# Optimization experiments

Measured on AMD Instinct MI355X. Metric: run time of the kernel, lower is better.

The kernel has to match this reference:

```python
import jax, jax.numpy as jnp
import numpy as np

N, E, B = 20000, 320000, 64
HID, DEPTH, NFREQ = 128, 4, 8
NODE_DIM, EDGE_DIM, SG = 4, 3, 230
TWO_PI = 2.0 * np.pi


def setup_inputs() -> dict:
    key = jax.random.key(0)
    ks = jax.random.split(key, 20)
    inp = {}
    inp["x"] = jax.random.normal(ks[0], (N, NODE_DIM), jnp.float32)
    inp["edge_index"] = jax.random.randint(ks[1], (2, E), 0, N)
    inp["edge_attr"] = jax.random.normal(ks[2], (E, EDGE_DIM), jnp.float32)
    inp["batch"] = jnp.sort(jax.random.randint(ks[3], (N,), 0, B))
    inp["space_group"] = jax.random.randint(ks[4], (B,), 0, SG)
    inp["node_w"] = jax.random.normal(ks[5], (NODE_DIM, HID), jnp.float32) * 0.1
    inp["node_b"] = jnp.zeros((HID,), jnp.float32)
    inp["sg_table"] = jax.random.normal(ks[6], (SG, HID), jnp.float32) * 0.1
    inp["lin_w"] = jax.random.normal(ks[7], (DEPTH, 2 * HID + EDGE_DIM, HID), jnp.float32) * 0.05
    inp["lin_b"] = jnp.zeros((DEPTH, HID), jnp.float32)
    inp["att_w"] = jax.random.normal(ks[8], (DEPTH, 2 * HID + EDGE_DIM), jnp.float32) * 0.05
    inp["att_b"] = jnp.zeros((DEPTH,), jnp.float32)
    inp["fk_w"] = jax.random.normal(ks[9], (DEPTH, NFREQ, HID, HID), jnp.float32) * 0.1
    inp["fk_b"] = jnp.zeros((DEPTH, HID), jnp.float32)
    inp["bn_g"] = jnp.ones((DEPTH, HID), jnp.float32)
    inp["bn_b"] = jnp.zeros((DEPTH, HID), jnp.float32)
    inp["pool_w"] = jax.random.normal(ks[10], (HID,), jnp.float32) * 0.1
    inp["pool_b"] = jnp.zeros((), jnp.float32)
    inp["head_w1"] = jax.random.normal(ks[11], (4, 2 * HID, HID), jnp.float32) * 0.05
    inp["head_b1"] = jnp.zeros((4, HID), jnp.float32)
    for i, (nm, od) in enumerate([("e", 1), ("s", 3), ("c", 7), ("m", 3)]):
        inp[nm + "_w2"] = jax.random.normal(ks[12 + i], (HID, od), jnp.float32) * 0.05
        inp[nm + "_b2"] = jnp.zeros((od,), jnp.float32)
    return inp


def reference(x, edge_index, edge_attr, batch, space_group, node_w, node_b, sg_table,
              lin_w, lin_b, att_w, att_b, fk_w, fk_b, bn_g, bn_b, pool_w, pool_b,
              head_w1, head_b1, e_w2, e_b2, s_w2, s_b2, c_w2, c_b2, m_w2, m_b2):
    src, dst = edge_index[0], edge_index[1]  # x_j = x[src], x_i = x[dst]
    h = x @ node_w + node_b                  # [N, HID]
    sg = sg_table[space_group]               # [B, HID]
    freqs = jnp.arange(1, NFREQ + 1, dtype=h.dtype)
    for l in range(DEPTH):
        # edge conv: gather-concat-linear-sigmoid attention-scatter add
        tmp = jnp.concatenate([h[dst], h[src], edge_attr], axis=-1)   # [E, 2H+3]
        alpha = jax.nn.sigmoid(tmp @ att_w[l] + att_b[l])[:, None]    # [E, 1]
        msg = alpha * (tmp @ lin_w[l] + lin_b[l])                     # [E, H]
        h_conv = jax.ops.segment_sum(msg, dst, num_segments=N)
        # Fourier-Kolmogorov branch
        ang = TWO_PI * freqs[None, :, None] * h[:, None, :]           # [N, K, H]
        h_fk = (jnp.einsum('nki,kio->no', jnp.sin(ang), fk_w[l])
                + jnp.einsum('nki,kio->no', jnp.cos(ang), fk_w[l]) + fk_b[l])
        h = h_conv + h_fk
        # BatchNorm1d (batch statistics, training semantics) + ReLU; dropout = identity (eval)
        mu = h.mean(axis=0)
        var = h.var(axis=0)
        h = (h - mu) / jnp.sqrt(var + 1e-5) * bn_g[l] + bn_b[l]
        h = jax.nn.relu(h)
    # attention pool: softmax over ALL nodes (dim=0), as in the original
    a = jax.nn.softmax(h @ pool_w + pool_b, axis=0)[:, None]          # [N, 1]
    pooled = jax.ops.segment_sum(a * h, batch, num_segments=B)        # [B, H]
    comb = jnp.concatenate([pooled, sg], axis=-1)                     # [B, 2H]

    def head(i, w2, b2):
        z = jax.nn.relu(comb @ head_w1[i] + head_b1[i])
        return z @ w2 + b2

    energy = head(0, e_w2, e_b2)          # [B, 1]
    stability = head(1, s_w2, s_b2)       # [B, 3]
    crystal_system = head(2, c_w2, c_b2)  # [B, 7]
    material_type = head(3, m_w2, m_b2)   # [B, 3]
    return energy, stability, crystal_system, material_type
```

## Files before the change

kernel.cpp:

```cpp
#include <hip/hip_runtime.h>
#include <math.h>

#define HID 128
#define DEPTH 4
#define PSPLIT 16
#define SMAXB 40

typedef _Float16 half8 __attribute__((ext_vector_type(8)));
typedef float f4 __attribute__((ext_vector_type(4)));

__global__ void k_wsplit(const float* __restrict__ fkw, _Float16* __restrict__ whi,
                         _Float16* __restrict__ wlo) {
    __shared__ float sh[64][65];
    int bid = blockIdx.x;
    int l = bid >> 5; int r = bid & 31; int kb = r >> 1; int nbk = r & 1;
    const float* W = fkw + (size_t)l * 131072;
    _Float16* Hl = whi + (size_t)l * 131072;
    _Float16* Ll = wlo + (size_t)l * 131072;
    int k0 = kb * 64, n0 = nbk * 64;
    for (int i = threadIdx.x; i < 4096; i += 256) {
        int kk = i >> 6, nn = i & 63;
        sh[kk][nn] = W[(k0 + kk) * HID + n0 + nn];
    }
    __syncthreads();
    for (int i = threadIdx.x; i < 4096; i += 256) {
        int nn = i >> 6, kk = i & 63;
        float w = sh[kk][nn];
        _Float16 hi = (_Float16)w;
        _Float16 lo = (_Float16)((w - (float)hi) * 2048.f);
        Hl[(n0 + nn) * 1024 + k0 + kk] = hi;
        Ll[(n0 + nn) * 1024 + k0 + kk] = lo;
    }
}

__global__ void k_wsplit2(const float* __restrict__ linw, _Float16* __restrict__ lwhi,
                          _Float16* __restrict__ lwlo) {
    __shared__ float sh[64][65];
    int bid = blockIdx.x;
    int l = bid >> 3; int r = bid & 7; int cb = r >> 1; int kb = r & 1;
    const float* W = linw + (size_t)l * 259 * HID;
    int c0 = cb * 64, k0 = kb * 64;
    const float* base = W + (size_t)((c0 >= 128) ? 128 : 0) * HID + (c0 & 127);
    for (int i = threadIdx.x; i < 4096; i += 256) {
        int kk = i >> 6, cc = i & 63;
        sh[kk][cc] = base[(size_t)(k0 + kk) * HID + cc];
    }
    __syncthreads();
    _Float16* Hl = lwhi + (size_t)l * 32768;
    _Float16* Ll = lwlo + (size_t)l * 32768;
    for (int i = threadIdx.x; i < 4096; i += 256) {
        int cc = i >> 6, kk = i & 63;
        float w = sh[kk][cc];
        _Float16 hi = (_Float16)w;
        _Float16 lo = (_Float16)((w - (float)hi) * 2048.f);
        Hl[(size_t)(c0 + cc) * 128 + k0 + kk] = hi;
        Ll[(size_t)(c0 + cc) * 128 + k0 + kk] = lo;
    }
}

__global__ void k_hist(const int* __restrict__ dst, int* __restrict__ deg, int E) {
    int e = blockIdx.x * 256 + threadIdx.x;
    if (e < E) atomicAdd(&deg[dst[e]], 1);
}

__global__ void k_scan_a(const int* __restrict__ deg, int* __restrict__ bsum, int N) {
    __shared__ int sh[256];
    int i = blockIdx.x * 256 + threadIdx.x;
    sh[threadIdx.x] = (i < N) ? deg[i] : 0;
    __syncthreads();
    for (int off = 128; off > 0; off >>= 1) {
        if (threadIdx.x < (unsigned)off) sh[threadIdx.x] += sh[threadIdx.x + off];
        __syncthreads();
    }
    if (threadIdx.x == 0) bsum[blockIdx.x] = sh[0];
}

__global__ void k_scan_b(int* __restrict__ bsum, int nb) {
    __shared__ int sh[256];
    int v = (threadIdx.x < (unsigned)nb) ? bsum[threadIdx.x] : 0;
    sh[threadIdx.x] = v;
    __syncthreads();
    for (int off = 1; off < 256; off <<= 1) {
        int add = (threadIdx.x >= (unsigned)off) ? sh[threadIdx.x - off] : 0;
        __syncthreads();
        sh[threadIdx.x] += add;
        __syncthreads();
    }
    if (threadIdx.x < (unsigned)nb) bsum[threadIdx.x] = sh[threadIdx.x] - v;
}

__global__ void k_scan_c(const int* __restrict__ deg, const int* __restrict__ bsum,
                         int* __restrict__ offs, int* __restrict__ cursor, int N) {
    __shared__ int sh[256];
    int i = blockIdx.x * 256 + threadIdx.x;
    int v = (i < N) ? deg[i] : 0;
    sh[threadIdx.x] = v;
    __syncthreads();
    for (int off = 1; off < 256; off <<= 1) {
        int add = (threadIdx.x >= (unsigned)off) ? sh[threadIdx.x - off] : 0;
        __syncthreads();
        sh[threadIdx.x] += add;
        __syncthreads();
    }
    int ex = bsum[blockIdx.x] + sh[threadIdx.x] - v;
    if (i < N) { offs[i] = ex; cursor[i] = ex; }
    if (i == N - 1) offs[N] = ex + v;
}

__global__ void k_scatter(const int* __restrict__ src, const int* __restrict__ dst,
                          const float* __restrict__ ea, int* cursor,
                          int* __restrict__ srco, float4* __restrict__ ea3o, int E) {
    int e = blockIdx.x * 256 + threadIdx.x;
    if (e < E) {
        int d = dst[e];
        int p = atomicAdd(&cursor[d], 1);
        srco[p] = src[e];
        float4 q;
        q.x = ea[e * 3 + 0]; q.y = ea[e * 3 + 1]; q.z = ea[e * 3 + 2]; q.w = 0.f;
        ea3o[p] = q;
    }
}

__global__ void k_bstart(const int* __restrict__ batch, int* __restrict__ boffs, int N, int B) {
    int n = blockIdx.x * 256 + threadIdx.x;
    if (n >= N) return;
    int b1 = batch[n];
    if (n == 0) for (int b = 0; b <= b1; ++b) boffs[b] = 0;
    int b2 = (n + 1 < N) ? batch[n + 1] : B;
    for (int b = b1 + 1; b <= b2; ++b) boffs[b] = n + 1;
}

__global__ __launch_bounds__(512, 4) void k_nlgemm(const float* __restrict__ hsrc,
        const float* __restrict__ x, const float* __restrict__ nw, const float* __restrict__ nbv,
        const double* __restrict__ bnst, const float* __restrict__ bng, const float* __restrict__ bnb,
        int mode,
        const _Float16* __restrict__ lwhi, const _Float16* __restrict__ lwlo,
        const float* __restrict__ linb,
        const float* __restrict__ attw, const float* __restrict__ attb,
        float* __restrict__ A1, float* __restrict__ A2,
        float* __restrict__ a1, float* __restrict__ a2, int N) {
    __shared__ _Float16 ahi[32 * 128];
    __shared__ _Float16 alo[32 * 128];
    __shared__ float s_sc[128], s_sh[128];
    int tid = threadIdx.x;
    int nb = blockIdx.x * 32;
    if (mode == 1) {
        if (tid < 128) {
            double invN = 1.0 / (double)N;
            float mu = (float)(bnst[tid] * invN);
            float var = (float)(bnst[128 + tid] * invN) - mu * mu;
            float inv = 1.f / sqrtf(var + 1e-5f);
            float sc = bng[tid] * inv;
            s_sc[tid] = sc;
            s_sh[tid] = bnb[tid] - mu * sc;
        }
        __syncthreads();
    }
    {
        int row = tid >> 4;
        int o16 = tid & 15;
        int gn = nb + row;
        int rc = (gn < N) ? gn : (N - 1);
        float hv[8];
        if (mode == 0) {
            float4 xr = *(const float4*)&x[(size_t)rc * 4];
#pragma unroll
            for (int j = 0; j < 8; ++j) {
                int c = o16 * 8 + j;
                hv[j] = nbv[c] + xr.x * nw[c] + xr.y * nw[HID + c]
                       + xr.z * nw[2 * HID + c] + xr.w * nw[3 * HID + c];
            }
        } else {
            const float* hp = hsrc + (size_t)rc * HID + o16 * 8;
            *(float4*)&hv[0] = *(const float4*)hp;
            *(float4*)&hv[4] = *(const float4*)(hp + 4);
#pragma unroll
            for (int j = 0; j < 8; ++j) {
                int c = o16 * 8 + j;
                hv[j] = fmaxf(hv[j] * s_sc[c] + s_sh[c], 0.f);
            }
        }
        float p1 = 0.f, p2 = 0.f;
#pragma unroll
        for (int j = 0; j < 8; ++j) {
            int k = o16 * 8 + j;
            p1 += hv[j] * attw[k];
            p2 += hv[j] * attw[128 + k];
        }
        for (int off = 8; off > 0; off >>= 1) {
            p1 += __shfl_down(p1, off, 16);
            p2 += __shfl_down(p2, off, 16);
        }
        if (o16 == 0 && gn < N) {
            a1[gn] = p1 + attb[0];
            a2[gn] = p2;
        }
        int rs = row & 7;
        half8 vh, vl;
#pragma unroll
        for (int j = 0; j < 8; ++j) {
            float a = hv[j];
            _Float16 hi = (_Float16)a;
            vh[j] = hi;
            vl[j] = (_Float16)((a - (float)hi) * 2048.f);
        }
        int oct = o16 ^ rs;
        *(half8*)&ahi[row * 128 + oct * 8] = vh;
        *(half8*)&alo[row * 128 + oct * 8] = vl;
    }
    __syncthreads();
    int lane = tid & 63, wv = tid >> 6;
    int quad = lane >> 4, l16 = lane & 15;
    int n0 = wv * 32;
    f4 acc0[2][2], accL[2][2];
#pragma unroll
    for (int mi = 0; mi < 2; ++mi)
#pragma unroll
        for (int ni = 0; ni < 2; ++ni) { acc0[mi][ni] = (f4)(0.f); accL[mi][ni] = (f4)(0.f); }
    const _Float16* bhp0 = lwhi + (size_t)(n0 + l16) * 128 + quad * 8;
    const _Float16* bhp1 = lwhi + (size_t)(n0 + 16 + l16) * 128 + quad * 8;
    const _Float16* blp0 = lwlo + (size_t)(n0 + l16) * 128 + quad * 8;
    const _Float16* blp1 = lwlo + (size_t)(n0 + 16 + l16) * 128 + quad * 8;
    int rs16 = (l16 & 7) << 3;
#pragma unroll
    for (int step = 0; step < 4; ++step) {
        int ka = (step * 32 + quad * 8) ^ rs16;
        int ko = step * 32;
        half8 bh0 = *(const half8*)(bhp0 + ko);
        half8 bh1 = *(const half8*)(bhp1 + ko);
        half8 bl0 = *(const half8*)(blp0 + ko);
        half8 bl1 = *(const half8*)(blp1 + ko);
        half8 ah[2], al[2];
#pragma unroll
        for (int mi = 0; mi < 2; ++mi) {
            ah[mi] = *(const half8*)&ahi[(l16 + mi * 16) * 128 + ka];
            al[mi] = *(const half8*)&alo[(l16 + mi * 16) * 128 + ka];
        }
#pragma unroll
        for (int mi = 0; mi < 2; ++mi) {
            acc0[mi][0] = __builtin_amdgcn_mfma_f32_16x16x32_f16(ah[mi], bh0, acc0[mi][0], 0, 0, 0);
            acc0[mi][1] = __builtin_amdgcn_mfma_f32_16x16x32_f16(ah[mi], bh1, acc0[mi][1], 0, 0, 0);
            accL[mi][0] = __builtin_amdgcn_mfma_f32_16x16x32_f16(ah[mi], bl0, accL[mi][0], 0, 0, 0);
            accL[mi][1] = __builtin_amdgcn_mfma_f32_16x16x32_f16(ah[mi], bl1, accL[mi][1], 0, 0, 0);
            accL[mi][0] = __builtin_amdgcn_mfma_f32_16x16x32_f16(al[mi], bh0, accL[mi][0], 0, 0, 0);
            accL[mi][1] = __builtin_amdgcn_mfma_f32_16x16x32_f16(al[mi], bh1, accL[mi][1], 0, 0, 0);
        }
    }
    const float inv = 1.0f / 2048.0f;
#pragma unroll
    for (int mi = 0; mi < 2; ++mi)
#pragma unroll
        for (int ni = 0; ni < 2; ++ni)
#pragma unroll
            for (int r = 0; r < 4; ++r) {
                int gn = nb + mi * 16 + quad * 4 + r;
                if (gn >= N) continue;
                int cp = n0 + ni * 16 + l16;
                float val = acc0[mi][ni][r] + accL[mi][ni][r] * inv;
                if (cp < 128) A1[(size_t)gn * HID + cp] = val + linb[cp];
                else          A2[(size_t)gn * HID + cp - 128] = val;
            }
}

__global__ __launch_bounds__(256) void k_edge(const float* __restrict__ A1,
        const float* __restrict__ A2, const float* __restrict__ a1,
        const float* __restrict__ a2, const int* __restrict__ srco,
        const float4* __restrict__ ea3o, const int* __restrict__ offs,
        const float* __restrict__ linw3, const float* __restrict__ attw3,
        float* __restrict__ hconv, int N) {
    __shared__ float part[8][HID + 4];
    int n = blockIdx.x;
    int tid = threadIdx.x;
    int lane32 = tid & 31, slot = tid >> 5;
    int c4 = lane32 * 4;
    float4 w0v = *(const float4*)&linw3[c4];
    float4 w1v = *(const float4*)&linw3[HID + c4];
    float4 w2v = *(const float4*)&linw3[2 * HID + c4];
    float aw0 = attw3[0], aw1 = attw3[1], aw2 = attw3[2];
    float a1n = a1[n];
    float4 A1v = *(const float4*)&A1[(size_t)n * HID + c4];
    float4 acc; acc.x = acc.y = acc.z = acc.w = 0.f;
    int s0 = offs[n], s1 = offs[n + 1];
    for (int idx = s0 + slot; idx < s1; idx += 8) {
        int s = srco[idx];
        float4 q = ea3o[idx];
        float logit = a1n + a2[s] + q.x * aw0 + q.y * aw1 + q.z * aw2;
        float al = 1.f / (1.f + __expf(-logit));
        float4 a2v = *(const float4*)&A2[(size_t)s * HID + c4];
        float4 pre;
        pre.x = A1v.x + a2v.x + q.x * w0v.x + q.y * w1v.x + q.z * w2v.x;
        pre.y = A1v.y + a2v.y + q.x * w0v.y + q.y * w1v.y + q.z * w2v.y;
        pre.z = A1v.z + a2v.z + q.x * w0v.z + q.y * w1v.z + q.z * w2v.z;
        pre.w = A1v.w + a2v.w + q.x * w0v.w + q.y * w1v.w + q.z * w2v.w;
        acc.x += al * pre.x; acc.y += al * pre.y;
        acc.z += al * pre.z; acc.w += al * pre.w;
    }
    *(float4*)&part[slot][c4] = acc;
    __syncthreads();
    if (slot == 0) {
        float4 p = *(const float4*)&part[0][c4];
#pragma unroll
        for (int s = 1; s < 8; ++s) {
            float4 r = *(const float4*)&part[s][c4];
            p.x += r.x; p.y += r.y; p.z += r.z; p.w += r.w;
        }
        *(float4*)&hconv[(size_t)n * HID + c4] = p;
    }
}

#define FK_MT 64
__global__ __launch_bounds__(512, 4) void k_fk(const float* __restrict__ hsrc,
        const float* __restrict__ x, const float* __restrict__ nw, const float* __restrict__ nbv,
        const double* __restrict__ bnst, const float* __restrict__ bng, const float* __restrict__ bnb,
        int mode,
        const _Float16* __restrict__ whi, const _Float16* __restrict__ wlo,
        float* __restrict__ p0, float* __restrict__ p1,
        float* __restrict__ p2, float* __restrict__ p3, int N) {
    __shared__ _Float16 ahi[FK_MT * 256];
    __shared__ _Float16 alo[FK_MT * 256];
    __shared__ float s_sc[128], s_sh[128];
    int tid = threadIdx.x;
    int bx = blockIdx.x;
    int nb = (bx >> 2) * FK_MT;
    int ks = bx & 3;
    int kbase = ks * 256;
    int fr0 = kbase >> 7;
    if (mode == 1) {
        if (tid < 128) {
            double invN = 1.0 / (double)N;
            float mu = (float)(bnst[tid] * invN);
            float var = (float)(bnst[128 + tid] * invN) - mu * mu;
            float inv = 1.f / sqrtf(var + 1e-5f);
            float sc = bng[tid] * inv;
            s_sc[tid] = sc;
            s_sh[tid] = bnb[tid] - mu * sc;
        }
        __syncthreads();
    }
    {
        int row = tid >> 3;
        int o8 = tid & 7;
        int gn = nb + row;
        int rc = (gn < N) ? gn : (N - 1);
        float hv[2][8];
        if (mode == 0) {
            float4 xr = *(const float4*)&x[(size_t)rc * 4];
#pragma unroll
            for (int s = 0; s < 2; ++s)
#pragma unroll
                for (int j = 0; j < 8; ++j) {
                    int c = s * 64 + o8 * 8 + j;
                    hv[s][j] = nbv[c] + xr.x * nw[c] + xr.y * nw[HID + c]
                              + xr.z * nw[2 * HID + c] + xr.w * nw[3 * HID + c];
                }
        } else {
            const float* hp = hsrc + (size_t)rc * HID + o8 * 8;
            *(float4*)&hv[0][0] = *(const float4*)hp;
            *(float4*)&hv[0][4] = *(const float4*)(hp + 4);
            *(float4*)&hv[1][0] = *(const float4*)(hp + 64);
            *(float4*)&hv[1][4] = *(const float4*)(hp + 68);
#pragma unroll
            for (int s = 0; s < 2; ++s)
#pragma unroll
                for (int j = 0; j < 8; ++j) {
                    int c = s * 64 + o8 * 8 + j;
                    hv[s][j] = fmaxf(hv[s][j] * s_sc[c] + s_sh[c], 0.f);
                }
        }
        int rs = row & 7;
#pragma unroll
        for (int g = 0; g < 2; ++g) {
            float freqf = 6.2831853f * (float)(fr0 + g + 1);
#pragma unroll
            for (int s = 0; s < 2; ++s) {
                half8 vh, vl;
#pragma unroll
                for (int j = 0; j < 8; ++j) {
                    float ang = freqf * hv[s][j] + 0.78539816f;
                    float a = 1.41421356f * __sinf(ang);
                    _Float16 hi = (_Float16)a;
                    vh[j] = hi;
                    vl[j] = (_Float16)((a - (float)hi) * 2048.f);
                }
                int oct = (g * 16 + s * 8 + o8) ^ rs;
                *(half8*)&ahi[row * 256 + oct * 8] = vh;
                *(half8*)&alo[row * 256 + oct * 8] = vl;
            }
        }
    }
    __syncthreads();
    int lane = tid & 63, wv = tid >> 6;
    int quad = lane >> 4, l16 = lane & 15;
    int n0w = wv * 16;
    f4 acc0[4], accL[4];
#pragma unroll
    for (int mi = 0; mi < 4; ++mi) { acc0[mi] = (f4)(0.f); accL[mi] = (f4)(0.f); }
    const _Float16* bhp = whi + (size_t)(n0w + l16) * 1024 + kbase + quad * 8;
    const _Float16* blp = wlo + (size_t)(n0w + l16) * 1024 + kbase + quad * 8;
    int rs16 = (l16 & 7) << 3;
#pragma unroll 2
    for (int step = 0; step < 8; ++step) {
        int ka = (step * 32 + quad * 8) ^ rs16;
        int ko = step * 32;
        half8 bh = *(const half8*)(bhp + ko);
        half8 bl = *(const half8*)(blp + ko);
        half8 ah[4], al[4];
#pragma unroll
        for (int mi = 0; mi < 4; ++mi) {
            ah[mi] = *(const half8*)&ahi[(l16 + mi * 16) * 256 + ka];
            al[mi] = *(const half8*)&alo[(l16 + mi * 16) * 256 + ka];
        }
#pragma unroll
        for (int mi = 0; mi < 4; ++mi) {
            acc0[mi] = __builtin_amdgcn_mfma_f32_16x16x32_f16(ah[mi], bh, acc0[mi], 0, 0, 0);
            accL[mi] = __builtin_amdgcn_mfma_f32_16x16x32_f16(ah[mi], bl, accL[mi], 0, 0, 0);
            accL[mi] = __builtin_amdgcn_mfma_f32_16x16x32_f16(al[mi], bh, accL[mi], 0, 0, 0);
        }
    }
    float* p = (ks == 0) ? p0 : (ks == 1) ? p1 : (ks == 2) ? p2 : p3;
    const float inv = 1.0f / 2048.0f;
#pragma unroll
    for (int mi = 0; mi < 4; ++mi)
#pragma unroll
        for (int r = 0; r < 4; ++r) {
            int gn = nb + mi * 16 + quad * 4 + r;
            if (gn < N)
                p[gn * HID + n0w + l16] = acc0[mi][r] + accL[mi][r] * inv;
        }
}

__global__ __launch_bounds__(256) void k_bn_stats(float* __restrict__ hconv,
                           const float* __restrict__ p0, const float* __restrict__ p1,
                           const float* __restrict__ p2, const float* __restrict__ p3,
                           const float* __restrict__ fkb,
                           double* __restrict__ stats, int N) {
    int tid = threadIdx.x;
    int cq = tid & 31, rg = tid >> 5;
    int c4 = cq * 4;
    float4 bias = *(const float4*)&fkb[c4];
    float s1[4] = {0, 0, 0, 0}, s2[4] = {0, 0, 0, 0};
    for (int n = blockIdx.x * 8 + rg; n < N; n += gridDim.x * 8) {
        size_t idx = (size_t)n * HID + c4;
        float4 a  = *(const float4*)&hconv[idx];
        float4 b0 = *(const float4*)&p0[idx];
        float4 b1 = *(const float4*)&p1[idx];
        float4 b2 = *(const float4*)&p2[idx];
        float4 b3 = *(const float4*)&p3[idx];
        float4 v;
        v.x = a.x + b0.x + b1.x + b2.x + b3.x + bias.x;
        v.y = a.y + b0.y + b1.y + b2.y + b3.y + bias.y;
        v.z = a.z + b0.z + b1.z + b2.z + b3.z + bias.z;
        v.w = a.w + b0.w + b1.w + b2.w + b3.w + bias.w;
        *(float4*)&hconv[idx] = v;
        s1[0] += v.x; s2[0] += v.x * v.x;
        s1[1] += v.y; s2[1] += v.y * v.y;
        s1[2] += v.z; s2[2] += v.z * v.z;
        s1[3] += v.w; s2[3] += v.w * v.w;
    }
#pragma unroll
    for (int j = 0; j < 4; ++j) {
        s1[j] += __shfl_down(s1[j], 32);
        s2[j] += __shfl_down(s2[j], 32);
    }
    __shared__ float sh1[4][32][4], sh2[4][32][4];
    int wv = tid >> 6, lane = tid & 63;
    if (lane < 32) {
#pragma unroll
        for (int j = 0; j < 4; ++j) { sh1[wv][lane][j] = s1[j]; sh2[wv][lane][j] = s2[j]; }
    }
    __syncthreads();
    if (tid < 128) {
        int cq2 = tid >> 2, j2 = tid & 3;
        float t1 = sh1[0][cq2][j2] + sh1[1][cq2][j2] + sh1[2][cq2][j2] + sh1[3][cq2][j2];
        float t2 = sh2[0][cq2][j2] + sh2[1][cq2][j2] + sh2[2][cq2][j2] + sh2[3][cq2][j2];
        int c = cq2 * 4 + j2;
        atomicAdd(&stats[c], (double)t1);
        atomicAdd(&stats[128 + c], (double)t2);
    }
}

__global__ void k_bn_apply(const float* __restrict__ hsum, const double* __restrict__ stats,
                           const float* __restrict__ g, const float* __restrict__ b,
                           const float* __restrict__ pw, const float* __restrict__ pb,
                           float* __restrict__ h, float* __restrict__ s,
                           int do_score, int N) {
    int idx = blockIdx.x * 256 + threadIdx.x;
    int row = idx >> 5, cq = idx & 31;
    int c4 = cq * 4;
    int valid = row < N;
    double invN = 1.0 / (double)N;
    float p = 0.f;
    if (valid) {
        float4 hv = *(const float4*)&hsum[(size_t)row * HID + c4];
        float vin[4] = {hv.x, hv.y, hv.z, hv.w};
        float4 ov;
        float* po = &ov.x;
#pragma unroll
        for (int j = 0; j < 4; ++j) {
            int c = c4 + j;
            float mu = (float)(stats[c] * invN);
            float var = (float)(stats[128 + c] * invN) - mu * mu;
            float inv = 1.f / sqrtf(var + 1e-5f);
            float sc = g[c] * inv;
            float sh = b[c] - mu * sc;
            float oo = fmaxf(vin[j] * sc + sh, 0.f);
            po[j] = oo;
            if (do_score) p += oo * pw[c];
        }
        *(float4*)&h[(size_t)row * HID + c4] = ov;
    }
    if (do_score) {
        for (int off = 16; off > 0; off >>= 1) p += __shfl_down(p, off, 32);
        if ((threadIdx.x & 31) == 0 && valid) s[row] = p + pb[0];
    }
}

__global__ void k_smax1(const float* __restrict__ s, float* __restrict__ mzp, int N) {
    __shared__ float red[256];
    float m = -INFINITY;
    for (int n = blockIdx.x * 256 + threadIdx.x; n < N; n += SMAXB * 256)
        m = fmaxf(m, s[n]);
    red[threadIdx.x] = m;
    __syncthreads();
    for (int off = 128; off > 0; off >>= 1) {
        if (threadIdx.x < (unsigned)off)
            red[threadIdx.x] = fmaxf(red[threadIdx.x], red[threadIdx.x + off]);
        __syncthreads();
    }
    m = red[0];
    __syncthreads();
    float z = 0.f;
    for (int n = blockIdx.x * 256 + threadIdx.x; n < N; n += SMAXB * 256)
        z += __expf(s[n] - m);
    red[threadIdx.x] = z;
    __syncthreads();
    for (int off = 128; off > 0; off >>= 1) {
        if (threadIdx.x < (unsigned)off) red[threadIdx.x] += red[threadIdx.x + off];
        __syncthreads();
    }
    if (threadIdx.x == 0) { mzp[blockIdx.x * 2] = m; mzp[blockIdx.x * 2 + 1] = red[0]; }
}

__device__ __forceinline__ void combine_mz(const float* mzp, float& m, float& Z) {
    m = -INFINITY;
#pragma unroll 8
    for (int i = 0; i < SMAXB; ++i) m = fmaxf(m, mzp[i * 2]);
    Z = 0.f;
#pragma unroll 8
    for (int i = 0; i < SMAXB; ++i) Z += mzp[i * 2 + 1] * __expf(mzp[i * 2] - m);
}

__global__ void k_pool_part(const float* __restrict__ h, const float* __restrict__ s,
                            const float* __restrict__ mzp, const int* __restrict__ boffs,
                            float* __restrict__ part) {
    int b = blockIdx.x >> 4, split = blockIdx.x & (PSPLIT - 1);
    int c = threadIdx.x & 127, half = threadIdx.x >> 7;
    float m, Z;
    combine_mz(mzp, m, Z);
    (void)Z;
    int n0 = boffs[b], n1 = boffs[b + 1];
    float acc = 0.f;
    for (int n = n0 + split * 2 + half; n < n1; n += PSPLIT * 2)
        acc += __expf(s[n] - m) * h[n * HID + c];
    __shared__ float prt[2][HID];
    prt[half][c] = acc;
    __syncthreads();
    if (half == 0) part[(size_t)(b * PSPLIT + split) * HID + c] = prt[0][c] + prt[1][c];
}

__global__ void k_pool_sum(const float* __restrict__ part, const float* __restrict__ mzp,
                           float* __restrict__ pooled) {
    int b = blockIdx.x, c = threadIdx.x;
    float m, Z;
    combine_mz(mzp, m, Z);
    float acc = 0.f;
#pragma unroll
    for (int i = 0; i < PSPLIT; ++i) acc += part[(size_t)(b * PSPLIT + i) * HID + c];
    pooled[b * HID + c] = acc / Z;
}

__global__ __launch_bounds__(256) void k_head(const float* __restrict__ pooled,
                       const float* __restrict__ sg_table,
                       const int* __restrict__ space_group,
                       const float* __restrict__ hw1, const float* __restrict__ hb1,
                       const float* __restrict__ ew2, const float* __restrict__ eb2,
                       const float* __restrict__ sw2, const float* __restrict__ sb2,
                       const float* __restrict__ cw2, const float* __restrict__ cb2,
                       const float* __restrict__ mw2, const float* __restrict__ mb2,
                       float* __restrict__ out, int B) {
    __shared__ float comb[256];
    __shared__ float zred[2][128];
    __shared__ float zsh[128];
    int b = blockIdx.x >> 2, i = blockIdx.x & 3;
    int t = threadIdx.x;
    comb[t] = (t < 128) ? pooled[b * HID + t] : sg_table[space_group[b] * HID + (t - 128)];
    __syncthreads();
    int half = t >> 7, tt = t & 127;
    const float* W = hw1 + ((size_t)i * 256 + half * 128) * HID;
    const float* cb = &comb[half * 128];
    float z = 0.f;
#pragma unroll 8
    for (int k = 0; k < 128; ++k) z += cb[k] * W[k * HID + tt];
    zred[half][tt] = z;
    __syncthreads();
    if (t < 128) zsh[t] = fmaxf(zred[0][t] + zred[1][t] + hb1[i * HID + t], 0.f);
    __syncthreads();
    const int od[4] = {1, 3, 7, 3};
    const int base[4] = {0, 64, 256, 704};
    const float* w2 = (i == 0) ? ew2 : (i == 1) ? sw2 : (i == 2) ? cw2 : mw2;
    const float* b2 = (i == 0) ? eb2 : (i == 1) ? sb2 : (i == 2) ? cb2 : mb2;
    int odi = od[i];
    if (t < odi) {
        float o = b2[t];
        for (int c = 0; c < HID; ++c) o += zsh[c] * w2[c * odi + t];
        out[base[i] + b * odi + t] = o;
    }
}

extern "C" void kernel_launch(void* const* d_in, const int* in_sizes, int n_in,
                              void* d_out, int out_size, void* d_ws, size_t ws_size,
                              hipStream_t stream) {
    const float* x          = (const float*)d_in[0];
    const int*   edge_index = (const int*)d_in[1];
    const float* edge_attr  = (const float*)d_in[2];
    const int*   batch      = (const int*)d_in[3];
    const int*   space_group= (const int*)d_in[4];
    const float* node_w     = (const float*)d_in[5];
    const float* node_b     = (const float*)d_in[6];
    const float* sg_table   = (const float*)d_in[7];
    const float* lin_w      = (const float*)d_in[8];
    const float* lin_b      = (const float*)d_in[9];
    const float* att_w      = (const float*)d_in[10];
    const float* att_b      = (const float*)d_in[11];
    const float* fk_w       = (const float*)d_in[12];
    const float* fk_b       = (const float*)d_in[13];
    const float* bn_g       = (const float*)d_in[14];
    const float* bn_b       = (const float*)d_in[15];
    const float* pool_w     = (const float*)d_in[16];
    const float* pool_b     = (const float*)d_in[17];
    const float* head_w1    = (const float*)d_in[18];
    const float* head_b1    = (const float*)d_in[19];
    const float* ew2 = (const float*)d_in[20]; const float* eb2 = (const float*)d_in[21];
    const float* sw2 = (const float*)d_in[22]; const float* sb2 = (const float*)d_in[23];
    const float* cw2 = (const float*)d_in[24]; const float* cb2 = (const float*)d_in[25];
    const float* mw2 = (const float*)d_in[26]; const float* mb2 = (const float*)d_in[27];
    float* out = (float*)d_out;

    const int N = in_sizes[3];
    const int E = in_sizes[1] / 2;
    const int B = in_sizes[4];
    const int* src = edge_index;
    const int* dst = edge_index + E;

    char* w = (char*)d_ws;
    auto alloc = [&](size_t bytes) { char* p = w; w += (bytes + 255) & ~(size_t)255; return p; };
    float*  h      = (float*)alloc((size_t)N * HID * 4);
    float*  A1     = (float*)alloc((size_t)N * HID * 4);
    float*  A2     = (float*)alloc((size_t)N * HID * 4);
    float*  p2     = (float*)alloc((size_t)N * HID * 4);
    float*  p3     = (float*)alloc((size_t)N * HID * 4);
    float*  hcv0   = (float*)alloc((size_t)N * HID * 4);
    float*  hcv1   = (float*)alloc((size_t)N * HID * 4);
    float*  a1     = (float*)alloc((size_t)N * 4);
    float*  a2     = (float*)alloc((size_t)N * 4);
    float*  sbuf   = (float*)alloc((size_t)N * 4);
    int*    deg    = (int*)alloc((size_t)N * 4);
    int*    cursor = (int*)alloc((size_t)N * 4);
    int*    offs   = (int*)alloc((size_t)(N + 1) * 4);
    int*    srco   = (int*)alloc((size_t)E * 4);
    float4* ea3o   = (float4*)alloc((size_t)E * 16);
    _Float16* whi  = (_Float16*)alloc((size_t)DEPTH * 1024 * HID * 2);
    _Float16* wlo  = (_Float16*)alloc((size_t)DEPTH * 1024 * HID * 2);
    _Float16* lwhi = (_Float16*)alloc((size_t)DEPTH * 256 * HID * 2);
    _Float16* lwlo = (_Float16*)alloc((size_t)DEPTH * 256 * HID * 2);
    int*    bsum   = (int*)alloc(256 * 4);
    int*    boffs  = (int*)alloc((size_t)(B + 1) * 4);
    double* stats  = (double*)alloc((size_t)DEPTH * 256 * 8);
    float*  mzp    = (float*)alloc(SMAXB * 2 * 4);
    float*  part   = (float*)alloc((size_t)B * PSPLIT * HID * 4);
    float*  pooled = (float*)alloc((size_t)B * HID * 4);

    const int nchunk = (N + 255) / 256;
    const int echunk = (E + 255) / 256;

    k_wsplit<<<128, 256, 0, stream>>>(fk_w, whi, wlo);
    k_wsplit2<<<32, 256, 0, stream>>>(lin_w, lwhi, lwlo);
    hipMemsetAsync(deg, 0, (size_t)N * 4, stream);
    hipMemsetAsync(stats, 0, (size_t)DEPTH * 256 * 8, stream);
    k_hist<<<echunk, 256, 0, stream>>>(dst, deg, E);
    k_scan_a<<<nchunk, 256, 0, stream>>>(deg, bsum, N);
    k_scan_b<<<1, 256, 0, stream>>>(bsum, nchunk);
    k_scan_c<<<nchunk, 256, 0, stream>>>(deg, bsum, offs, cursor, N);
    k_scatter<<<echunk, 256, 0, stream>>>(src, dst, edge_attr, cursor, srco, ea3o, E);
    k_bstart<<<nchunk, 256, 0, stream>>>(batch, boffs, N, B);

    float* hcv[2] = {hcv0, hcv1};
    for (int l = 0; l < DEPTH; ++l) {
        const float* linw_l = lin_w + (size_t)l * 259 * HID;
        int mode = (l == 0) ? 0 : 1;
        const double* bst = (l == 0) ? (const double*)nullptr : stats + (size_t)(l - 1) * 256;
        const float* bgl = bn_g + (size_t)((l == 0) ? 0 : (l - 1)) * HID;
        const float* bbl = bn_b + (size_t)((l == 0) ? 0 : (l - 1)) * HID;
        const float* hprev = (l == 0) ? h : hcv[(l - 1) & 1];
        float* hcur = hcv[l & 1];
        k_nlgemm<<<(N + 31) / 32, 512, 0, stream>>>(
            hprev, x, node_w, node_b, bst, bgl, bbl, mode,
            lwhi + (size_t)l * 32768, lwlo + (size_t)l * 32768,
            lin_b + l * HID, att_w + (size_t)l * 259, att_b + l,
            A1, A2, a1, a2, N);
        k_edge<<<N, 256, 0, stream>>>(A1, A2, a1, a2, srco, ea3o, offs,
                                      linw_l + 256 * HID, att_w + (size_t)l * 259 + 256,
                                      hcur, N);
        k_fk<<<((N + FK_MT - 1) / FK_MT) * 4, 512, 0, stream>>>(
            hprev, x, node_w, node_b, bst, bgl, bbl, mode,
            whi + (size_t)l * 131072, wlo + (size_t)l * 131072, A1, A2, p2, p3, N);
        k_bn_stats<<<320, 256, 0, stream>>>(hcur, A1, A2, p2, p3, fk_b + l * HID,
                                            stats + (size_t)l * 256, N);
    }
    k_bn_apply<<<(N * 32 + 255) / 256, 256, 0, stream>>>(
        hcv[(DEPTH - 1) & 1], stats + (size_t)(DEPTH - 1) * 256,
        bn_g + (size_t)(DEPTH - 1) * HID, bn_b + (size_t)(DEPTH - 1) * HID,
        pool_w, pool_b, h, sbuf, 1, N);

    k_smax1<<<SMAXB, 256, 0, stream>>>(sbuf, mzp, N);
    k_pool_part<<<B * PSPLIT, 256, 0, stream>>>(h, sbuf, mzp, boffs, part);
    k_pool_sum<<<B, 128, 0, stream>>>(part, mzp, pooled);
    k_head<<<B * 4, 256, 0, stream>>>(pooled, sg_table, space_group, head_w1, head_b1,
                                      ew2, eb2, sw2, sb2, cw2, cb2, mw2, mb2, out, B);
}
```

Measured before the change: 650.9 us.

## Merge Fourier-kernel and linear GEMMs into one launch; fold pool_sum into head

The Fourier-kernel GEMM (k_fk) and the node linear GEMM (k_nlgemm) now run in a single kernel, k_gemms, with blockIdx ranges selecting each role. The FK partial outputs go to new buffers q0/q1 instead of reusing A1/A2, so the FK work can run before k_edge rather than after it. This removes one launch per layer and lets the two independent GEMMs fill the GPU together. The final k_pool_sum is folded into k_head, which saves another launch. In exchange the shared-memory footprint of the linear-GEMM blocks grows to the FK size, which may lower occupancy, and two extra N×HID buffers are used.

```diff
diff --git a/kernel.cpp b/kernel.cpp
--- a/kernel.cpp
+++ b/kernel.cpp
@@ -130,20 +130,24 @@
     for (int b = b1 + 1; b <= b2; ++b) boffs[b] = n + 1;
 }
 
-__global__ __launch_bounds__(512, 4) void k_nlgemm(const float* __restrict__ hsrc,
+#define FK_MT 64
+__global__ __launch_bounds__(512, 4) void k_gemms(const float* __restrict__ hsrc,
         const float* __restrict__ x, const float* __restrict__ nw, const float* __restrict__ nbv,
         const double* __restrict__ bnst, const float* __restrict__ bng, const float* __restrict__ bnb,
         int mode,
+        const _Float16* __restrict__ whi, const _Float16* __restrict__ wlo,
+        float* __restrict__ q0, float* __restrict__ q1,
+        float* __restrict__ p2, float* __restrict__ p3,
         const _Float16* __restrict__ lwhi, const _Float16* __restrict__ lwlo,
         const float* __restrict__ linb,
         const float* __restrict__ attw, const float* __restrict__ attb,
         float* __restrict__ A1, float* __restrict__ A2,
-        float* __restrict__ a1, float* __restrict__ a2, int N) {
-    __shared__ _Float16 ahi[32 * 128];
-    __shared__ _Float16 alo[32 * 128];
+        float* __restrict__ a1, float* __restrict__ a2,
+        int FKB, int N) {
+    __shared__ _Float16 ahi[FK_MT * 256];
+    __shared__ _Float16 alo[FK_MT * 256];
     __shared__ float s_sc[128], s_sh[128];
     int tid = threadIdx.x;
-    int nb = blockIdx.x * 32;
     if (mode == 1) {
         if (tid < 128) {
             double invN = 1.0 / (double)N;
@@ -156,110 +160,209 @@
         }
         __syncthreads();
     }
-    {
-        int row = tid >> 4;
-        int o16 = tid & 15;
-        int gn = nb + row;
-        int rc = (gn < N) ? gn : (N - 1);
-        float hv[8];
-        if (mode == 0) {
-            float4 xr = *(const float4*)&x[(size_t)rc * 4];
-#pragma unroll
-            for (int j = 0; j < 8; ++j) {
-                int c = o16 * 8 + j;
-                hv[j] = nbv[c] + xr.x * nw[c] + xr.y * nw[HID + c]
-                       + xr.z * nw[2 * HID + c] + xr.w * nw[3 * HID + c];
-            }
-        } else {
-            const float* hp = hsrc + (size_t)rc * HID + o16 * 8;
-            *(float4*)&hv[0] = *(const float4*)hp;
-            *(float4*)&hv[4] = *(const float4*)(hp + 4);
-#pragma unroll
-            for (int j = 0; j < 8; ++j) {
-                int c = o16 * 8 + j;
-                hv[j] = fmaxf(hv[j] * s_sc[c] + s_sh[c], 0.f);
+    if (blockIdx.x < (unsigned)FKB) {
+        int bx = blockIdx.x;
+        int nb = (bx >> 2) * FK_MT;
+        int ks = bx & 3;
+        int kbase = ks * 256;
+        int fr0 = kbase >> 7;
+        {
+            int row = tid >> 3;
+            int o8 = tid & 7;
+            int gn = nb + row;
+            int rc = (gn < N) ? gn : (N - 1);
+            float hv[2][8];
+            if (mode == 0) {
+                float4 xr = *(const float4*)&x[(size_t)rc * 4];
+#pragma unroll
+                for (int s = 0; s < 2; ++s)
+#pragma unroll
+                    for (int j = 0; j < 8; ++j) {
+                        int c = s * 64 + o8 * 8 + j;
+                        hv[s][j] = nbv[c] + xr.x * nw[c] + xr.y * nw[HID + c]
+                                  + xr.z * nw[2 * HID + c] + xr.w * nw[3 * HID + c];
+                    }
+            } else {
+                const float* hp = hsrc + (size_t)rc * HID + o8 * 8;
+                *(float4*)&hv[0][0] = *(const float4*)hp;
+                *(float4*)&hv[0][4] = *(const float4*)(hp + 4);
+                *(float4*)&hv[1][0] = *(const float4*)(hp + 64);
+                *(float4*)&hv[1][4] = *(const float4*)(hp + 68);
+#pragma unroll
+                for (int s = 0; s < 2; ++s)
+#pragma unroll
+                    for (int j = 0; j < 8; ++j) {
+                        int c = s * 64 + o8 * 8 + j;
+                        hv[s][j] = fmaxf(hv[s][j] * s_sc[c] + s_sh[c], 0.f);
+                    }
+            }
+            int rs = row & 7;
+#pragma unroll
+            for (int g = 0; g < 2; ++g) {
+                float freqf = 6.2831853f * (float)(fr0 + g + 1);
+#pragma unroll
+                for (int s = 0; s < 2; ++s) {
+                    half8 vh, vl;
+#pragma unroll
+                    for (int j = 0; j < 8; ++j) {
+                        float ang = freqf * hv[s][j] + 0.78539816f;
+                        float a = 1.41421356f * __sinf(ang);
+                        _Float16 hi = (_Float16)a;
+                        vh[j] = hi;
+                        vl[j] = (_Float16)((a - (float)hi) * 2048.f);
+                    }
+                    int oct = (g * 16 + s * 8 + o8) ^ rs;
+                    *(half8*)&ahi[row * 256 + oct * 8] = vh;
+                    *(half8*)&alo[row * 256 + oct * 8] = vl;
+                }
             }
         }
-        float p1 = 0.f, p2 = 0.f;
-#pragma unroll
-        for (int j = 0; j < 8; ++j) {
-            int k = o16 * 8 + j;
-            p1 += hv[j] * attw[k];
-            p2 += hv[j] * attw[128 + k];
+        __syncthreads();
+        int lane = tid & 63, wv = tid >> 6;
+        int quad = lane >> 4, l16 = lane & 15;
+        int n0w = wv * 16;
+        f4 acc0[4], accL[4];
+#pragma unroll
+        for (int mi = 0; mi < 4; ++mi) { acc0[mi] = (f4)(0.f); accL[mi] = (f4)(0.f); }
+        const _Float16* bhp = whi + (size_t)(n0w + l16) * 1024 + kbase + quad * 8;
+        const _Float16* blp = wlo + (size_t)(n0w + l16) * 1024 + kbase + quad * 8;
+        int rs16 = (l16 & 7) << 3;
+#pragma unroll 2
+        for (int step = 0; step < 8; ++step) {
+            int ka = (step * 32 + quad * 8) ^ rs16;
+            int ko = step * 32;
+            half8 bh = *(const half8*)(bhp + ko);
+            half8 bl = *(const half8*)(blp + ko);
+            half8 ah[4], al[4];
+#pragma unroll
+            for (int mi = 0; mi < 4; ++mi) {
+                ah[mi] = *(const half8*)&ahi[(l16 + mi * 16) * 256 + ka];
+                al[mi] = *(const half8*)&alo[(l16 + mi * 16) * 256 + ka];
+            }
+#pragma unroll
+            for (int mi = 0; mi < 4; ++mi) {
+                acc0[mi] = __builtin_amdgcn_mfma_f32_16x16x32_f16(ah[mi], bh, acc0[mi], 0, 0, 0);
+                accL[mi] = __builtin_amdgcn_mfma_f32_16x16x32_f16(ah[mi], bl, accL[mi], 0, 0, 0);
+                accL[mi] = __builtin_amdgcn_mfma_f32_16x16x32_f16(al[mi], bh, accL[mi], 0, 0, 0);
+            }
         }
-        for (int off = 8; off > 0; off >>= 1) {
-            p1 += __shfl_down(p1, off, 16);
-            p2 += __shfl_down(p2, off, 16);
-        }
-        if (o16 == 0 && gn < N) {
-            a1[gn] = p1 + attb[0];
-            a2[gn] = p2;
-        }
-        int rs = row & 7;
-        half8 vh, vl;
-#pragma unroll
-        for (int j = 0; j < 8; ++j) {
-            float a = hv[j];
-            _Float16 hi = (_Float16)a;
-            vh[j] = hi;
-            vl[j] = (_Float16)((a - (float)hi) * 2048.f);
-        }
-        int oct = o16 ^ rs;
-        *(half8*)&ahi[row * 128 + oct * 8] = vh;
-        *(half8*)&alo[row * 128 + oct * 8] = vl;
-    }
-    __syncthreads();
-    int lane = tid & 63, wv = tid >> 6;
-    int quad = lane >> 4, l16 = lane & 15;
-    int n0 = wv * 32;
-    f4 acc0[2][2], accL[2][2];
-#pragma unroll
-    for (int mi = 0; mi < 2; ++mi)
-#pragma unroll
-        for (int ni = 0; ni < 2; ++ni) { acc0[mi][ni] = (f4)(0.f); accL[mi][ni] = (f4)(0.f); }
-    const _Float16* bhp0 = lwhi + (size_t)(n0 + l16) * 128 + quad * 8;
-    const _Float16* bhp1 = lwhi + (size_t)(n0 + 16 + l16) * 128 + quad * 8;
-    const _Float16* blp0 = lwlo + (size_t)(n0 + l16) * 128 + quad * 8;
-    const _Float16* blp1 = lwlo + (size_t)(n0 + 16 + l16) * 128 + quad * 8;
-    int rs16 = (l16 & 7) << 3;
-#pragma unroll
-    for (int step = 0; step < 4; ++step) {
-        int ka = (step * 32 + quad * 8) ^ rs16;
-        int ko = step * 32;
-        half8 bh0 = *(const half8*)(bhp0 + ko);
-        half8 bh1 = *(const half8*)(bhp1 + ko);
-        half8 bl0 = *(const half8*)(blp0 + ko);
-        half8 bl1 = *(const half8*)(blp1 + ko);
-        half8 ah[2], al[2];
-#pragma unroll
-        for (int mi = 0; mi < 2; ++mi) {
-            ah[mi] = *(const half8*)&ahi[(l16 + mi * 16) * 128 + ka];
-            al[mi] = *(const half8*)&alo[(l16 + mi * 16) * 128 + ka];
-        }
-#pragma unroll
-        for (int mi = 0; mi < 2; ++mi) {
-            acc0[mi][0] = __builtin_amdgcn_mfma_f32_16x16x32_f16(ah[mi], bh0, acc0[mi][0], 0, 0, 0);
-            acc0[mi][1] = __builtin_amdgcn_mfma_f32_16x16x32_f16(ah[mi], bh1, acc0[mi][1], 0, 0, 0);
-            accL[mi][0] = __builtin_amdgcn_mfma_f32_16x16x32_f16(ah[mi], bl0, accL[mi][0], 0, 0, 0);
-            accL[mi][1] = __builtin_amdgcn_mfma_f32_16x16x32_f16(ah[mi], bl1, accL[mi][1], 0, 0, 0);
-            accL[mi][0] = __builtin_amdgcn_mfma_f32_16x16x32_f16(al[mi], bh0, accL[mi][0], 0, 0, 0);
-            accL[mi][1] = __builtin_amdgcn_mfma_f32_16x16x32_f16(al[mi], bh1, accL[mi][1], 0, 0, 0);
-        }
-    }
-    const float inv = 1.0f / 2048.0f;
-#pragma unroll
-    for (int mi = 0; mi < 2; ++mi)
-#pragma unroll
-        for (int ni = 0; ni < 2; ++ni)
+        float* p = (ks == 0) ? q0 : (ks == 1) ? q1 : (ks == 2) ? p2 : p3;
+        const float inv = 1.0f / 2048.0f;
+#pragma unroll
+        for (int mi = 0; mi < 4; ++mi)
 #pragma unroll
             for (int r = 0; r < 4; ++r) {
                 int gn = nb + mi * 16 + quad * 4 + r;
-                if (gn >= N) continue;
-                int cp = n0 + ni * 16 + l16;
-                float val = acc0[mi][ni][r] + accL[mi][ni][r] * inv;
-                if (cp < 128) A1[(size_t)gn * HID + cp] = val + linb[cp];
-                else          A2[(size_t)gn * HID + cp - 128] = val;
-            }
+                if (gn < N)
+                    p[gn * HID + n0w + l16] = acc0[mi][r] + accL[mi][r] * inv;
+            }
+    } else {
+        int nb = (blockIdx.x - FKB) * 32;
+        {
+            int row = tid >> 4;
+            int o16 = tid & 15;
+            int gn = nb + row;
+            int rc = (gn < N) ? gn : (N - 1);
+            float hv[8];
+            if (mode == 0) {
+                float4 xr = *(const float4*)&x[(size_t)rc * 4];
+#pragma unroll
+                for (int j = 0; j < 8; ++j) {
+                    int c = o16 * 8 + j;
+                    hv[j] = nbv[c] + xr.x * nw[c] + xr.y * nw[HID + c]
+                           + xr.z * nw[2 * HID + c] + xr.w * nw[3 * HID + c];
+                }
+            } else {
+                const float* hp = hsrc + (size_t)rc * HID + o16 * 8;
+                *(float4*)&hv[0] = *(const float4*)hp;
+                *(float4*)&hv[4] = *(const float4*)(hp + 4);
+#pragma unroll
+                for (int j = 0; j < 8; ++j) {
+                    int c = o16 * 8 + j;
+                    hv[j] = fmaxf(hv[j] * s_sc[c] + s_sh[c], 0.f);
+                }
+            }
+            float p1 = 0.f, p2d = 0.f;
+#pragma unroll
+            for (int j = 0; j < 8; ++j) {
+                int k = o16 * 8 + j;
+                p1 += hv[j] * attw[k];
+                p2d += hv[j] * attw[128 + k];
+            }
+            for (int off = 8; off > 0; off >>= 1) {
+                p1 += __shfl_down(p1, off, 16);
+                p2d += __shfl_down(p2d, off, 16);
+            }
+            if (o16 == 0 && gn < N) {
+                a1[gn] = p1 + attb[0];
+                a2[gn] = p2d;
+            }
+            int rs = row & 7;
+            half8 vh, vl;
+#pragma unroll
+            for (int j = 0; j < 8; ++j) {
+                float a = hv[j];
+                _Float16 hi = (_Float16)a;
+                vh[j] = hi;
+                vl[j] = (_Float16)((a - (float)hi) * 2048.f);
+            }
+            int oct = o16 ^ rs;
+            *(half8*)&ahi[row * 128 + oct * 8] = vh;
+            *(half8*)&alo[row * 128 + oct * 8] = vl;
+        }
+        __syncthreads();
+        int lane = tid & 63, wv = tid >> 6;
+        int quad = lane >> 4, l16 = lane & 15;
+        int n0 = wv * 32;
+        f4 acc0[2][2], accL[2][2];
+#pragma unroll
+        for (int mi = 0; mi < 2; ++mi)
+#pragma unroll
+            for (int ni = 0; ni < 2; ++ni) { acc0[mi][ni] = (f4)(0.f); accL[mi][ni] = (f4)(0.f); }
+        const _Float16* bhp0 = lwhi + (size_t)(n0 + l16) * 128 + quad * 8;
+        const _Float16* bhp1 = lwhi + (size_t)(n0 + 16 + l16) * 128 + quad * 8;
+        const _Float16* blp0 = lwlo + (size_t)(n0 + l16) * 128 + quad * 8;
+        const _Float16* blp1 = lwlo + (size_t)(n0 + 16 + l16) * 128 + quad * 8;
+        int rs16 = (l16 & 7) << 3;
+#pragma unroll
+        for (int step = 0; step < 4; ++step) {
+            int ka = (step * 32 + quad * 8) ^ rs16;
+            int ko = step * 32;
+            half8 bh0 = *(const half8*)(bhp0 + ko);
+            half8 bh1 = *(const half8*)(bhp1 + ko);
+            half8 bl0 = *(const half8*)(blp0 + ko);
+            half8 bl1 = *(const half8*)(blp1 + ko);
+            half8 ah[2], al[2];
+#pragma unroll
+            for (int mi = 0; mi < 2; ++mi) {
+                ah[mi] = *(const half8*)&ahi[(l16 + mi * 16) * 128 + ka];
+                al[mi] = *(const half8*)&alo[(l16 + mi * 16) * 128 + ka];
+            }
+#pragma unroll
+            for (int mi = 0; mi < 2; ++mi) {
+                acc0[mi][0] = __builtin_amdgcn_mfma_f32_16x16x32_f16(ah[mi], bh0, acc0[mi][0], 0, 0, 0);
+                acc0[mi][1] = __builtin_amdgcn_mfma_f32_16x16x32_f16(ah[mi], bh1, acc0[mi][1], 0, 0, 0);
+                accL[mi][0] = __builtin_amdgcn_mfma_f32_16x16x32_f16(ah[mi], bl0, accL[mi][0], 0, 0, 0);
+                accL[mi][1] = __builtin_amdgcn_mfma_f32_16x16x32_f16(ah[mi], bl1, accL[mi][1], 0, 0, 0);
+                accL[mi][0] = __builtin_amdgcn_mfma_f32_16x16x32_f16(al[mi], bh0, accL[mi][0], 0, 0, 0);
+                accL[mi][1] = __builtin_amdgcn_mfma_f32_16x16x32_f16(al[mi], bh1, accL[mi][1], 0, 0, 0);
+            }
+        }
+        const float inv = 1.0f / 2048.0f;
+#pragma unroll
+        for (int mi = 0; mi < 2; ++mi)
+#pragma unroll
+            for (int ni = 0; ni < 2; ++ni)
+#pragma unroll
+                for (int r = 0; r < 4; ++r) {
+                    int gn = nb + mi * 16 + quad * 4 + r;
+                    if (gn >= N) continue;
+                    int cp = n0 + ni * 16 + l16;
+                    float val = acc0[mi][ni][r] + accL[mi][ni][r] * inv;
+                    if (cp < 128) A1[(size_t)gn * HID + cp] = val + linb[cp];
+                    else          A2[(size_t)gn * HID + cp - 128] = val;
+                }
+    }
 }
 
 __global__ __launch_bounds__(256) void k_edge(const float* __restrict__ A1,
@@ -308,127 +411,6 @@
     }
 }
 
-#define FK_MT 64
-__global__ __launch_bounds__(512, 4) void k_fk(const float* __restrict__ hsrc,
-        const float* __restrict__ x, const float* __restrict__ nw, const float* __restrict__ nbv,
-        const double* __restrict__ bnst, const float* __restrict__ bng, const float* __restrict__ bnb,
-        int mode,
-        const _Float16* __restrict__ whi, const _Float16* __restrict__ wlo,
-        float* __restrict__ p0, float* __restrict__ p1,
-        float* __restrict__ p2, float* __restrict__ p3, int N) {
-    __shared__ _Float16 ahi[FK_MT * 256];
-    __shared__ _Float16 alo[FK_MT * 256];
-    __shared__ float s_sc[128], s_sh[128];
-    int tid = threadIdx.x;
-    int bx = blockIdx.x;
-    int nb = (bx >> 2) * FK_MT;
-    int ks = bx & 3;
-    int kbase = ks * 256;
-    int fr0 = kbase >> 7;
-    if (mode == 1) {
-        if (tid < 128) {
-            double invN = 1.0 / (double)N;
-            float mu = (float)(bnst[tid] * invN);
-            float var = (float)(bnst[128 + tid] * invN) - mu * mu;
-            float inv = 1.f / sqrtf(var + 1e-5f);
-            float sc = bng[tid] * inv;
-            s_sc[tid] = sc;
-            s_sh[tid] = bnb[tid] - mu * sc;
-        }
-        __syncthreads();
-    }
-    {
-        int row = tid >> 3;
-        int o8 = tid & 7;
-        int gn = nb + row;
-        int rc = (gn < N) ? gn : (N - 1);
-        float hv[2][8];
-        if (mode == 0) {
-            float4 xr = *(const float4*)&x[(size_t)rc * 4];
-#pragma unroll
-            for (int s = 0; s < 2; ++s)
-#pragma unroll
-                for (int j = 0; j < 8; ++j) {
-                    int c = s * 64 + o8 * 8 + j;
-                    hv[s][j] = nbv[c] + xr.x * nw[c] + xr.y * nw[HID + c]
-                              + xr.z * nw[2 * HID + c] + xr.w * nw[3 * HID + c];
-                }
-        } else {
-            const float* hp = hsrc + (size_t)rc * HID + o8 * 8;
-            *(float4*)&hv[0][0] = *(const float4*)hp;
-            *(float4*)&hv[0][4] = *(const float4*)(hp + 4);
-            *(float4*)&hv[1][0] = *(const float4*)(hp + 64);
-            *(float4*)&hv[1][4] = *(const float4*)(hp + 68);
-#pragma unroll
-            for (int s = 0; s < 2; ++s)
-#pragma unroll
-                for (int j = 0; j < 8; ++j) {
-                    int c = s * 64 + o8 * 8 + j;
-                    hv[s][j] = fmaxf(hv[s][j] * s_sc[c] + s_sh[c], 0.f);
-                }
-        }
-        int rs = row & 7;
-#pragma unroll
-        for (int g = 0; g < 2; ++g) {
-            float freqf = 6.2831853f * (float)(fr0 + g + 1);
-#pragma unroll
-            for (int s = 0; s < 2; ++s) {
-                half8 vh, vl;
-#pragma unroll
-                for (int j = 0; j < 8; ++j) {
-                    float ang = freqf * hv[s][j] + 0.78539816f;
-                    float a = 1.41421356f * __sinf(ang);
-                    _Float16 hi = (_Float16)a;
-                    vh[j] = hi;
-                    vl[j] = (_Float16)((a - (float)hi) * 2048.f);
-                }
-                int oct = (g * 16 + s * 8 + o8) ^ rs;
-                *(half8*)&ahi[row * 256 + oct * 8] = vh;
-                *(half8*)&alo[row * 256 + oct * 8] = vl;
-            }
-        }
-    }
-    __syncthreads();
-    int lane = tid & 63, wv = tid >> 6;
-    int quad = lane >> 4, l16 = lane & 15;
-    int n0w = wv * 16;
-    f4 acc0[4], accL[4];
-#pragma unroll
-    for (int mi = 0; mi < 4; ++mi) { acc0[mi] = (f4)(0.f); accL[mi] = (f4)(0.f); }
-    const _Float16* bhp = whi + (size_t)(n0w + l16) * 1024 + kbase + quad * 8;
-    const _Float16* blp = wlo + (size_t)(n0w + l16) * 1024 + kbase + quad * 8;
-    int rs16 = (l16 & 7) << 3;
-#pragma unroll 2
-    for (int step = 0; step < 8; ++step) {
-        int ka = (step * 32 + quad * 8) ^ rs16;
-        int ko = step * 32;
-        half8 bh = *(const half8*)(bhp + ko);
-        half8 bl = *(const half8*)(blp + ko);
-        half8 ah[4], al[4];
-#pragma unroll
-        for (int mi = 0; mi < 4; ++mi) {
-            ah[mi] = *(const half8*)&ahi[(l16 + mi * 16) * 256 + ka];
-            al[mi] = *(const half8*)&alo[(l16 + mi * 16) * 256 + ka];
-        }
-#pragma unroll
-        for (int mi = 0; mi < 4; ++mi) {
-            acc0[mi] = __builtin_amdgcn_mfma_f32_16x16x32_f16(ah[mi], bh, acc0[mi], 0, 0, 0);
-            accL[mi] = __builtin_amdgcn_mfma_f32_16x16x32_f16(ah[mi], bl, accL[mi], 0, 0, 0);
-            accL[mi] = __builtin_amdgcn_mfma_f32_16x16x32_f16(al[mi], bh, accL[mi], 0, 0, 0);
-        }
-    }
-    float* p = (ks == 0) ? p0 : (ks == 1) ? p1 : (ks == 2) ? p2 : p3;
-    const float inv = 1.0f / 2048.0f;
-#pragma unroll
-    for (int mi = 0; mi < 4; ++mi)
-#pragma unroll
-        for (int r = 0; r < 4; ++r) {
-            int gn = nb + mi * 16 + quad * 4 + r;
-            if (gn < N)
-                p[gn * HID + n0w + l16] = acc0[mi][r] + accL[mi][r] * inv;
-        }
-}
-
 __global__ __launch_bounds__(256) void k_bn_stats(float* __restrict__ hconv,
                            const float* __restrict__ p0, const float* __restrict__ p1,
                            const float* __restrict__ p2, const float* __restrict__ p3,
@@ -568,18 +550,8 @@
     if (half == 0) part[(size_t)(b * PSPLIT + split) * HID + c] = prt[0][c] + prt[1][c];
 }
 
-__global__ void k_pool_sum(const float* __restrict__ part, const float* __restrict__ mzp,
-                           float* __restrict__ pooled) {
-    int b = blockIdx.x, c = threadIdx.x;
-    float m, Z;
-    combine_mz(mzp, m, Z);
-    float acc = 0.f;
-#pragma unroll
-    for (int i = 0; i < PSPLIT; ++i) acc += part[(size_t)(b * PSPLIT + i) * HID + c];
-    pooled[b * HID + c] = acc / Z;
-}
-
-__global__ __launch_bounds__(256) void k_head(const float* __restrict__ pooled,
+__global__ __launch_bounds__(256) void k_head(const float* __restrict__ part,
+                       const float* __restrict__ mzp,
                        const float* __restrict__ sg_table,
                        const int* __restrict__ space_group,
                        const float* __restrict__ hw1, const float* __restrict__ hb1,
@@ -593,7 +565,16 @@
     __shared__ float zsh[128];
     int b = blockIdx.x >> 2, i = blockIdx.x & 3;
     int t = threadIdx.x;
-    comb[t] = (t < 128) ? pooled[b * HID + t] : sg_table[space_group[b] * HID + (t - 128)];
+    if (t < 128) {
+        float m, Z;
+        combine_mz(mzp, m, Z);
+        float acc = 0.f;
+#pragma unroll
+        for (int j = 0; j < PSPLIT; ++j) acc += part[(size_t)(b * PSPLIT + j) * HID + t];
+        comb[t] = acc / Z;
+    } else {
+        comb[t] = sg_table[space_group[b] * HID + (t - 128)];
+    }
     __syncthreads();
     int half = t >> 7, tt = t & 127;
     const float* W = hw1 + ((size_t)i * 256 + half * 128) * HID;
@@ -657,6 +638,8 @@
     float*  h      = (float*)alloc((size_t)N * HID * 4);
     float*  A1     = (float*)alloc((size_t)N * HID * 4);
     float*  A2     = (float*)alloc((size_t)N * HID * 4);
+    float*  q0     = (float*)alloc((size_t)N * HID * 4);
+    float*  q1     = (float*)alloc((size_t)N * HID * 4);
     float*  p2     = (float*)alloc((size_t)N * HID * 4);
     float*  p3     = (float*)alloc((size_t)N * HID * 4);
     float*  hcv0   = (float*)alloc((size_t)N * HID * 4);
@@ -678,10 +661,11 @@
     double* stats  = (double*)alloc((size_t)DEPTH * 256 * 8);
     float*  mzp    = (float*)alloc(SMAXB * 2 * 4);
     float*  part   = (float*)alloc((size_t)B * PSPLIT * HID * 4);
-    float*  pooled = (float*)alloc((size_t)B * HID * 4);
 
     const int nchunk = (N + 255) / 256;
     const int echunk = (E + 255) / 256;
+    const int FKB = ((N + FK_MT - 1) / FK_MT) * 4;
+    const int NLB = (N + 31) / 32;
 
     k_wsplit<<<128, 256, 0, stream>>>(fk_w, whi, wlo);
     k_wsplit2<<<32, 256, 0, stream>>>(lin_w, lwhi, lwlo);
@@ -703,18 +687,16 @@
         const float* bbl = bn_b + (size_t)((l == 0) ? 0 : (l - 1)) * HID;
         const float* hprev = (l == 0) ? h : hcv[(l - 1) & 1];
         float* hcur = hcv[l & 1];
-        k_nlgemm<<<(N + 31) / 32, 512, 0, stream>>>(
+        k_gemms<<<FKB + NLB, 512, 0, stream>>>(
             hprev, x, node_w, node_b, bst, bgl, bbl, mode,
+            whi + (size_t)l * 131072, wlo + (size_t)l * 131072, q0, q1, p2, p3,
             lwhi + (size_t)l * 32768, lwlo + (size_t)l * 32768,
             lin_b + l * HID, att_w + (size_t)l * 259, att_b + l,
-            A1, A2, a1, a2, N);
+            A1, A2, a1, a2, FKB, N);
         k_edge<<<N, 256, 0, stream>>>(A1, A2, a1, a2, srco, ea3o, offs,
                                       linw_l + 256 * HID, att_w + (size_t)l * 259 + 256,
                                       hcur, N);
-        k_fk<<<((N + FK_MT - 1) / FK_MT) * 4, 512, 0, stream>>>(
-            hprev, x, node_w, node_b, bst, bgl, bbl, mode,
-            whi + (size_t)l * 131072, wlo + (size_t)l * 131072, A1, A2, p2, p3, N);
-        k_bn_stats<<<320, 256, 0, stream>>>(hcur, A1, A2, p2, p3, fk_b + l * HID,
+        k_bn_stats<<<320, 256, 0, stream>>>(hcur, q0, q1, p2, p3, fk_b + l * HID,
                                             stats + (size_t)l * 256, N);
     }
     k_bn_apply<<<(N * 32 + 255) / 256, 256, 0, stream>>>(
@@ -724,7 +706,6 @@
 
     k_smax1<<<SMAXB, 256, 0, stream>>>(sbuf, mzp, N);
     k_pool_part<<<B * PSPLIT, 256, 0, stream>>>(h, sbuf, mzp, boffs, part);
-    k_pool_sum<<<B, 128, 0, stream>>>(part, mzp, pooled);
-    k_head<<<B * 4, 256, 0, stream>>>(pooled, sg_table, space_group, head_w1, head_b1,
+    k_head<<<B * 4, 256, 0, stream>>>(part, mzp, sg_table, space_group, head_w1, head_b1,
                                       ew2, eb2, sw2, sb2, cw2, cb2, mw2, mb2, out, B);
 }
```

After: 625.7 us. 1.04x faster.
